# Kernel optimization log

Hardware: AMD Instinct MI355X
Metric: run time of the kernel (lower is better)

## Reference

```python
import jax, jax.numpy as jnp
import numpy as np

N_NODES, N_EDGES, D_FEAT, D_HID, K_CHEB = 30000, 480000, 256, 256, 2


def setup_inputs() -> dict:
    N, E, D, H, K = N_NODES, N_EDGES, D_FEAT, D_HID, K_CHEB
    key = jax.random.key(0)
    ks = jax.random.split(key, 24)
    sD = 1.0 / np.sqrt(D)
    sH = 1.0 / np.sqrt(H)
    inp = {
        "x": jax.random.normal(ks[0], (N, D), jnp.float32),
        "edge_index": jax.random.randint(ks[1], (2, E), 0, N),
        "edge_weight": jax.random.uniform(ks[2], (E,), jnp.float32),
        "h": jax.random.normal(ks[3], (N, H), jnp.float32),
        "c": jax.random.normal(ks[4], (N, H), jnp.float32),
        "src_neighbor_ids": jax.random.randint(ks[5], (E,), 0, N),
        "dst_neighbor_ids": jax.random.randint(ks[6], (E,), 0, N),
    }
    for j, nm in enumerate(["W_i", "W_f", "W_g", "W_o"]):
        inp[nm] = jax.random.normal(ks[7 + j], (D, H), jnp.float32) * sD
    for j, nm in enumerate(["Wc_i", "Wc_f", "Wc_g", "Wc_o"]):
        inp[nm] = jax.random.normal(ks[11 + j], (K, H, H), jnp.float32) * sH
    for nm in ["bc_i", "bc_f", "bc_g", "bc_o", "b_i", "b_f", "b_g", "b_o", "b_lin"]:
        inp[nm] = jnp.zeros((H,), jnp.float32)
    for j, nm in enumerate(["w_ci", "w_cf", "w_co"]):
        inp[nm] = jax.random.normal(ks[15 + j], (H,), jnp.float32) * 0.1
    inp["W_lin"] = jax.random.normal(ks[18], (H, H), jnp.float32) * sH
    return inp


def _cheb_conv(h, src, dst, norm, W, b):
    # ChebConv, K=2, sym norm, lambda_max=2: T0 = h, T1 = L_hat h = -D^-1/2 A D^-1/2 h
    out = h @ W[0]
    t1 = jax.ops.segment_sum(norm[:, None] * h[src], dst, num_segments=h.shape[0])
    return out + t1 @ W[1] + b


def reference(x, edge_index, edge_weight, h, c, src_neighbor_ids, dst_neighbor_ids,
              W_i, W_f, W_g, W_o, Wc_i, Wc_f, Wc_g, Wc_o,
              bc_i, bc_f, bc_g, bc_o, w_ci, w_cf, w_co,
              b_i, b_f, b_g, b_o, W_lin, b_lin):
    src, dst = edge_index[0], edge_index[1]
    n = x.shape[0]
    # neighbor-feature augmentation: gather both BEFORE any update, then scatter-add
    snf = x[src_neighbor_ids]
    dnf = x[dst_neighbor_ids]
    x = x.at[src].add(snf)
    x = x.at[dst].add(dnf)
    # symmetric Chebyshev normalization (lambda_max = 2 -> diagonal of L_hat is 0)
    deg = jax.ops.segment_sum(edge_weight, src, num_segments=n)
    dinv = jnp.where(deg > 0, jax.lax.rsqrt(jnp.maximum(deg, 1e-12)), 0.0)
    norm = -dinv[src] * edge_weight * dinv[dst]
    # GCLSTM gates
    i = jax.nn.sigmoid(x @ W_i + _cheb_conv(h, src, dst, norm, Wc_i, bc_i) + w_ci * c + b_i)
    f = jax.nn.sigmoid(x @ W_f + _cheb_conv(h, src, dst, norm, Wc_f, bc_f) + w_cf * c + b_f)
    g = jnp.tanh(x @ W_g + _cheb_conv(h, src, dst, norm, Wc_g, bc_g) + b_g)
    c_new = f * c + i * g
    o = jax.nn.sigmoid(x @ W_o + _cheb_conv(h, src, dst, norm, Wc_o, bc_o) + w_co * c_new + b_o)
    h0 = o * jnp.tanh(c_new)
    h_out = jax.nn.relu(h0) @ W_lin + b_lin
    return (h_out, h0, c_new)
```

## Files before the change

kernel.cpp:

```cpp
#include <hip/hip_runtime.h>
#include <math.h>

#define NN 30000
#define NE 480000
#define DH 256
#define NH (NN * DH)
#define MPAD 30080
#define CAP 64

typedef _Float16 f16x4 __attribute__((ext_vector_type(4)));
typedef _Float16 f16x8 __attribute__((ext_vector_type(8)));
typedef float f32x4 __attribute__((ext_vector_type(4)));

static __device__ __forceinline__ float sigmoidf_(float x) {
    return 1.0f / (1.0f + __expf(-x));
}

static __device__ __forceinline__ void gload16(const _Float16* g, _Float16* l) {
    __builtin_amdgcn_global_load_lds(
        (const __attribute__((address_space(1))) void*)g,
        (__attribute__((address_space(3))) void*)l, 16, 0, 0);
}


__global__ void prep0(const int* __restrict__ src, const float* __restrict__ ew,
                      float* __restrict__ deg,
                      const float* __restrict__ x, _Float16* __restrict__ x16,
                      const float* __restrict__ h, _Float16* __restrict__ h16) {
    int b = blockIdx.x;
    if (b < 1875) {
        int e = b * 256 + threadIdx.x;
        if (e < NE) atomicAdd(&deg[src[e]], ew[e]);
        return;
    }
    int i = (b - 1875) * 256 + threadIdx.x;
    const int n8 = NN * 32;
    const float* in; _Float16* out; int idx;
    if (i < n8) { in = x; out = x16; idx = i; }
    else if (i < 2 * n8) { in = h; out = h16; idx = i - n8; }
    else return;
    const float4 p = *reinterpret_cast<const float4*>(&in[(size_t)idx * 8]);
    const float4 q = *reinterpret_cast<const float4*>(&in[(size_t)idx * 8 + 4]);
    f16x8 v;
    v[0] = (_Float16)p.x; v[1] = (_Float16)p.y; v[2] = (_Float16)p.z; v[3] = (_Float16)p.w;
    v[4] = (_Float16)q.x; v[5] = (_Float16)q.y; v[6] = (_Float16)q.z; v[7] = (_Float16)q.w;
    *reinterpret_cast<f16x8*>(&out[(size_t)idx * 8]) = v;
}

__global__ void dinv_kernel(float* __restrict__ deg) {
    int v = blockIdx.x * blockDim.x + threadIdx.x;
    if (v < NN) {
        float d = deg[v];
        deg[v] = (d > 0.0f) ? rsqrtf(fmaxf(d, 1e-12f)) : 0.0f;
    }
}

__global__ void scatter2(const int* __restrict__ src, const int* __restrict__ dst,
                         const int* __restrict__ snf, const int* __restrict__ dnf,
                         const float* __restrict__ w, const float* __restrict__ dinv,
                         int* __restrict__ cntS, int* __restrict__ cntD,
                         int* __restrict__ slotS, int2* __restrict__ slotD) {
    int e = blockIdx.x * blockDim.x + threadIdx.x;
    if (e >= NE) return;
    int s = src[e], d = dst[e];
    int pS = atomicAdd(&cntS[s], 1);
    if (pS < CAP) slotS[s * CAP + pS] = snf[e];
    float nrm = -dinv[s] * w[e] * dinv[d];
    int pD = atomicAdd(&cntD[d], 1);
    if (pD < CAP) slotD[d * CAP + pD] = make_int2(s | (dnf[e] << 15), __float_as_int(nrm));
}

__global__ __launch_bounds__(256) void fused_gather(const _Float16* __restrict__ x16,
                                                    const _Float16* __restrict__ h16,
                                                    const int* __restrict__ cntS,
                                                    const int* __restrict__ cntD,
                                                    const int4* __restrict__ slotS4,
                                                    const int4* __restrict__ slotD4,
                                                    _Float16* __restrict__ A16) {
    int wid = (blockIdx.x * blockDim.x + threadIdx.x) >> 6;
    int l = threadIdx.x & 63;
    if (wid >= MPAD) return;
    size_t rb = (size_t)wid * 768;
    if (wid >= NN) {
        f16x4 z = {};
        *reinterpret_cast<f16x4*>(&A16[rb + l * 4]) = z;
        *reinterpret_cast<f16x4*>(&A16[rb + 256 + l * 4]) = z;
        *reinterpret_cast<f16x4*>(&A16[rb + 512 + l * 4]) = z;
        return;
    }
    int nS = min(cntS[wid], CAP);
    int nD = min(cntD[wid], CAP);

    f16x4 xv = *reinterpret_cast<const f16x4*>(&x16[(size_t)wid * 256 + l * 4]);
    f16x4 hrow = *reinterpret_cast<const f16x4*>(&h16[(size_t)wid * 256 + l * 4]);
    float a0 = (float)xv[0], a1 = (float)xv[1], a2 = (float)xv[2], a3 = (float)xv[3];
    float t0 = 0.f, t1 = 0.f, t2 = 0.f, t3 = 0.f;

    const int4* pS = &slotS4[(size_t)wid * (CAP / 4)];
    for (int j = 0; j < nS; j += 4) {
        int4 e = pS[j >> 2];
        f16x4 v0, v1, v2, v3;
        v0 = *reinterpret_cast<const f16x4*>(&x16[(size_t)e.x * 256 + l * 4]);
        if (j + 1 < nS) v1 = *reinterpret_cast<const f16x4*>(&x16[(size_t)e.y * 256 + l * 4]);
        if (j + 2 < nS) v2 = *reinterpret_cast<const f16x4*>(&x16[(size_t)e.z * 256 + l * 4]);
        if (j + 3 < nS) v3 = *reinterpret_cast<const f16x4*>(&x16[(size_t)e.w * 256 + l * 4]);
        a0 += (float)v0[0]; a1 += (float)v0[1]; a2 += (float)v0[2]; a3 += (float)v0[3];
        if (j + 1 < nS) { a0 += (float)v1[0]; a1 += (float)v1[1]; a2 += (float)v1[2]; a3 += (float)v1[3]; }
        if (j + 2 < nS) { a0 += (float)v2[0]; a1 += (float)v2[1]; a2 += (float)v2[2]; a3 += (float)v2[3]; }
        if (j + 3 < nS) { a0 += (float)v3[0]; a1 += (float)v3[1]; a2 += (float)v3[2]; a3 += (float)v3[3]; }
    }

    const int4* pD = &slotD4[(size_t)wid * (CAP / 2)];
    for (int j = 0; j < nD; j += 4) {
        int4 ea = pD[(j >> 2) * 2];
        int4 eb = pD[(j >> 2) * 2 + 1];
        int p0 = ea.x, p1 = ea.z, p2 = eb.x, p3 = eb.z;
        float n0 = __int_as_float(ea.y), n1f = __int_as_float(ea.w);
        float n2f = __int_as_float(eb.y), n3f = __int_as_float(eb.w);
        f16x4 x0, x1, x2, x3, g0, g1, g2, g3;
        x0 = *reinterpret_cast<const f16x4*>(&x16[(size_t)(p0 >> 15) * 256 + l * 4]);
        g0 = *reinterpret_cast<const f16x4*>(&h16[(size_t)(p0 & 0x7fff) * 256 + l * 4]);
        if (j + 1 < nD) {
            x1 = *reinterpret_cast<const f16x4*>(&x16[(size_t)(p1 >> 15) * 256 + l * 4]);
            g1 = *reinterpret_cast<const f16x4*>(&h16[(size_t)(p1 & 0x7fff) * 256 + l * 4]);
        }
        if (j + 2 < nD) {
            x2 = *reinterpret_cast<const f16x4*>(&x16[(size_t)(p2 >> 15) * 256 + l * 4]);
            g2 = *reinterpret_cast<const f16x4*>(&h16[(size_t)(p2 & 0x7fff) * 256 + l * 4]);
        }
        if (j + 3 < nD) {
            x3 = *reinterpret_cast<const f16x4*>(&x16[(size_t)(p3 >> 15) * 256 + l * 4]);
            g3 = *reinterpret_cast<const f16x4*>(&h16[(size_t)(p3 & 0x7fff) * 256 + l * 4]);
        }
        a0 += (float)x0[0]; a1 += (float)x0[1]; a2 += (float)x0[2]; a3 += (float)x0[3];
        t0 += n0 * (float)g0[0]; t1 += n0 * (float)g0[1];
        t2 += n0 * (float)g0[2]; t3 += n0 * (float)g0[3];
        if (j + 1 < nD) {
            a0 += (float)x1[0]; a1 += (float)x1[1]; a2 += (float)x1[2]; a3 += (float)x1[3];
            t0 += n1f * (float)g1[0]; t1 += n1f * (float)g1[1];
            t2 += n1f * (float)g1[2]; t3 += n1f * (float)g1[3];
        }
        if (j + 2 < nD) {
            a0 += (float)x2[0]; a1 += (float)x2[1]; a2 += (float)x2[2]; a3 += (float)x2[3];
            t0 += n2f * (float)g2[0]; t1 += n2f * (float)g2[1];
            t2 += n2f * (float)g2[2]; t3 += n2f * (float)g2[3];
        }
        if (j + 3 < nD) {
            a0 += (float)x3[0]; a1 += (float)x3[1]; a2 += (float)x3[2]; a3 += (float)x3[3];
            t0 += n3f * (float)g3[0]; t1 += n3f * (float)g3[1];
            t2 += n3f * (float)g3[2]; t3 += n3f * (float)g3[3];
        }
    }

    f16x4 oX, oT;
    oX[0] = (_Float16)a0; oX[1] = (_Float16)a1; oX[2] = (_Float16)a2; oX[3] = (_Float16)a3;
    oT[0] = (_Float16)t0; oT[1] = (_Float16)t1; oT[2] = (_Float16)t2; oT[3] = (_Float16)t3;
    *reinterpret_cast<f16x4*>(&A16[rb + l * 4]) = oX;
    *reinterpret_cast<f16x4*>(&A16[rb + 256 + l * 4]) = hrow;
    *reinterpret_cast<f16x4*>(&A16[rb + 512 + l * 4]) = oT;
}


__global__ void wpack_kernel(const float* __restrict__ W_i, const float* __restrict__ W_f,
                             const float* __restrict__ W_g, const float* __restrict__ W_o,
                             const float* __restrict__ Wc_i, const float* __restrict__ Wc_f,
                             const float* __restrict__ Wc_g, const float* __restrict__ Wc_o,
                             const float* __restrict__ W_lin,
                             _Float16* __restrict__ WcatT, _Float16* __restrict__ WlinT) {
    int idx = blockIdx.x * blockDim.x + threadIdx.x;
    if (idx < 768 * 1024) {
        int k = idx >> 10, n = idx & 1023;
        int seg = k >> 8, kk = k & 255, gate = n >> 8, nn = n & 255;
        const float* p;
        if (seg == 0) {
            p = (gate == 0) ? W_i : (gate == 1) ? W_f : (gate == 2) ? W_g : W_o;
        } else {
            const float* base = (gate == 0) ? Wc_i : (gate == 1) ? Wc_f : (gate == 2) ? Wc_g : Wc_o;
            p = base + (seg - 1) * 65536;
        }
        WcatT[(size_t)n * 768 + k] = (_Float16)p[kk * 256 + nn];
    } else {
        int i2 = idx - 768 * 1024;
        if (i2 >= 256 * 256) return;
        int k = i2 >> 8, n = i2 & 255;
        WlinT[(size_t)n * 256 + k] = (_Float16)W_lin[k * 256 + n];
    }
}


template <int K, int N, bool HALF_OUT, bool SWZ1D>
__global__ __launch_bounds__(256) void gemm16(const _Float16* __restrict__ A,
                                              const _Float16* __restrict__ B,
                                              const float* __restrict__ bias,
                                              _Float16* __restrict__ outH,
                                              float* __restrict__ outF) {
    __shared__ _Float16 As[128 * 64];
    __shared__ _Float16 Bs[128 * 64];
    int tid = threadIdx.x;
    int w = tid >> 6, l = tid & 63;
    int wy = w >> 1, wx = w & 1;
    int bm, bn;
    if constexpr (SWZ1D) {
        constexpr int NT = N / 128;
        constexpr int TOT = (MPAD / 128) * NT;
        constexpr int CH = TOT / 8;
        int b = blockIdx.x;
        int v = (b & 7) * CH + (b >> 3);
        bm = (v / NT) * 128; bn = (v % NT) * 128;
    } else {
        bm = blockIdx.x * 128; bn = blockIdx.y * 128;
    }

    f32x4 acc[4][4];
    #pragma unroll
    for (int m = 0; m < 4; ++m)
        #pragma unroll
        for (int n = 0; n < 4; ++n)
            acc[m][n] = (f32x4){0.f, 0.f, 0.f, 0.f};

    int rowi = tid >> 3;
    int g = (tid & 7) ^ (rowi & 7);
    const _Float16* gA0 = A + (size_t)(bm + rowi) * K + g * 8;
    const _Float16* gB0 = B + (size_t)(bn + rowi) * K + g * 8;

    for (int kt = 0; kt < K; kt += 64) {
        #pragma unroll
        for (int i = 0; i < 4; ++i) {
            gload16(gA0 + kt + (size_t)i * 32 * K, &As[i * 2048 + w * 512]);
            gload16(gB0 + kt + (size_t)i * 32 * K, &Bs[i * 2048 + w * 512]);
        }
        __syncthreads();

        f16x8 af[4][2], bf[4][2];
        #pragma unroll
        for (int m = 0; m < 4; ++m) {
            int row = wy * 64 + m * 16 + (l & 15);
            #pragma unroll
            for (int ks = 0; ks < 2; ++ks) {
                int ch = (ks * 4 + (l >> 4)) ^ (l & 7);
                af[m][ks] = *reinterpret_cast<const f16x8*>(&As[row * 64 + ch * 8]);
            }
        }
        #pragma unroll
        for (int n = 0; n < 4; ++n) {
            int row = wx * 64 + n * 16 + (l & 15);
            #pragma unroll
            for (int ks = 0; ks < 2; ++ks) {
                int ch = (ks * 4 + (l >> 4)) ^ (l & 7);
                bf[n][ks] = *reinterpret_cast<const f16x8*>(&Bs[row * 64 + ch * 8]);
            }
        }
        #pragma unroll
        for (int ks = 0; ks < 2; ++ks)
            #pragma unroll
            for (int m = 0; m < 4; ++m)
                #pragma unroll
                for (int n = 0; n < 4; ++n)
                    acc[m][n] = __builtin_amdgcn_mfma_f32_16x16x32_f16(
                        af[m][ks], bf[n][ks], acc[m][n], 0, 0, 0);
        __syncthreads();
    }

    #pragma unroll
    for (int m = 0; m < 4; ++m) {
        #pragma unroll
        for (int n = 0; n < 4; ++n) {
            int col = bn + wx * 64 + n * 16 + (l & 15);
            #pragma unroll
            for (int j = 0; j < 4; ++j) {
                int row = bm + wy * 64 + m * 16 + (l >> 4) * 4 + j;
                if (row < NN) {
                    if constexpr (HALF_OUT)
                        outH[(size_t)row * N + col] = (_Float16)acc[m][n][j];
                    else
                        outF[(size_t)row * N + col] = acc[m][n][j] + bias[col];
                }
            }
        }
    }
}


__global__ void gate_kernel(const _Float16* __restrict__ pre, const float* __restrict__ c,
                            const float* __restrict__ bc_i, const float* __restrict__ bc_f,
                            const float* __restrict__ bc_g, const float* __restrict__ bc_o,
                            const float* __restrict__ b_i, const float* __restrict__ b_f,
                            const float* __restrict__ b_g, const float* __restrict__ b_o,
                            const float* __restrict__ w_ci, const float* __restrict__ w_cf,
                            const float* __restrict__ w_co,
                            float* __restrict__ h0p, float* __restrict__ cnp,
                            _Float16* __restrict__ relu16) {
    int idx = blockIdx.x * blockDim.x + threadIdx.x;
    if (idx >= MPAD * 64) return;
    int row = idx >> 6;
    int n4 = (idx & 63) << 2;
    if (row >= NN) {
        f16x4 z = {};
        *reinterpret_cast<f16x4*>(&relu16[(size_t)row * 256 + n4]) = z;
        return;
    }
    size_t pb = (size_t)row * 1024;
    f16x4 pi = *reinterpret_cast<const f16x4*>(&pre[pb + n4]);
    f16x4 pf = *reinterpret_cast<const f16x4*>(&pre[pb + 256 + n4]);
    f16x4 pg = *reinterpret_cast<const f16x4*>(&pre[pb + 512 + n4]);
    f16x4 po = *reinterpret_cast<const f16x4*>(&pre[pb + 768 + n4]);
    float4 cv = *reinterpret_cast<const float4*>(&c[(size_t)row * 256 + n4]);
    float4 vbci = *reinterpret_cast<const float4*>(&bc_i[n4]);
    float4 vbcf = *reinterpret_cast<const float4*>(&bc_f[n4]);
    float4 vbcg = *reinterpret_cast<const float4*>(&bc_g[n4]);
    float4 vbco = *reinterpret_cast<const float4*>(&bc_o[n4]);
    float4 vbi  = *reinterpret_cast<const float4*>(&b_i[n4]);
    float4 vbf  = *reinterpret_cast<const float4*>(&b_f[n4]);
    float4 vbg  = *reinterpret_cast<const float4*>(&b_g[n4]);
    float4 vbo  = *reinterpret_cast<const float4*>(&b_o[n4]);
    float4 vwci = *reinterpret_cast<const float4*>(&w_ci[n4]);
    float4 vwcf = *reinterpret_cast<const float4*>(&w_cf[n4]);
    float4 vwco = *reinterpret_cast<const float4*>(&w_co[n4]);
    const float* CV = (const float*)&cv;
    const float* BCI = (const float*)&vbci; const float* BCF = (const float*)&vbcf;
    const float* BCG = (const float*)&vbcg; const float* BCO = (const float*)&vbco;
    const float* BI = (const float*)&vbi;   const float* BF = (const float*)&vbf;
    const float* BG = (const float*)&vbg;   const float* BO = (const float*)&vbo;
    const float* WCI = (const float*)&vwci; const float* WCF = (const float*)&vwcf;
    const float* WCO = (const float*)&vwco;
    float4 cn4, h04;
    float* CN = (float*)&cn4; float* H0 = (float*)&h04;
    f16x4 rl;
    #pragma unroll
    for (int j = 0; j < 4; ++j) {
        float iv = sigmoidf_((float)pi[j] + BCI[j] + BI[j] + WCI[j] * CV[j]);
        float fv = sigmoidf_((float)pf[j] + BCF[j] + BF[j] + WCF[j] * CV[j]);
        float gv = tanhf((float)pg[j] + BCG[j] + BG[j]);
        float cn = fv * CV[j] + iv * gv;
        float ov = sigmoidf_((float)po[j] + BCO[j] + BO[j] + WCO[j] * cn);
        CN[j] = cn;
        float h0 = ov * tanhf(cn);
        H0[j] = h0;
        rl[j] = (_Float16)fmaxf(h0, 0.f);
    }
    *reinterpret_cast<float4*>(&cnp[(size_t)row * 256 + n4]) = cn4;
    *reinterpret_cast<float4*>(&h0p[(size_t)row * 256 + n4]) = h04;
    *reinterpret_cast<f16x4*>(&relu16[(size_t)row * 256 + n4]) = rl;
}


extern "C" void kernel_launch(void* const* d_in, const int* in_sizes, int n_in,
                              void* d_out, int out_size, void* d_ws, size_t ws_size,
                              hipStream_t stream) {
    const float* x   = (const float*)d_in[0];
    const int*   ei  = (const int*)d_in[1];
    const float* ew  = (const float*)d_in[2];
    const float* h   = (const float*)d_in[3];
    const float* c   = (const float*)d_in[4];
    const int*   snf = (const int*)d_in[5];
    const int*   dnf = (const int*)d_in[6];
    const float* W_i = (const float*)d_in[7];
    const float* W_f = (const float*)d_in[8];
    const float* W_g = (const float*)d_in[9];
    const float* W_o = (const float*)d_in[10];
    const float* Wc_i = (const float*)d_in[11];
    const float* Wc_f = (const float*)d_in[12];
    const float* Wc_g = (const float*)d_in[13];
    const float* Wc_o = (const float*)d_in[14];
    const float* bc_i = (const float*)d_in[15];
    const float* bc_f = (const float*)d_in[16];
    const float* bc_g = (const float*)d_in[17];
    const float* bc_o = (const float*)d_in[18];
    const float* b_i  = (const float*)d_in[19];
    const float* b_f  = (const float*)d_in[20];
    const float* b_g  = (const float*)d_in[21];
    const float* b_o  = (const float*)d_in[22];
    const float* b_lin = (const float*)d_in[23];
    const float* w_ci = (const float*)d_in[24];
    const float* w_cf = (const float*)d_in[25];
    const float* w_co = (const float*)d_in[26];
    const float* W_lin = (const float*)d_in[27];

    const int* src = ei;
    const int* dst = ei + NE;

    float* out = (float*)d_out;
    float* houtp = out;
    float* h0p   = out + NH;
    float* cnp   = out + 2 * NH;

    char* ws = (char*)d_ws;
    _Float16* pre16 = (_Float16*)ws;
    int* cntS = (int*)ws;
    int* cntD = (int*)(ws + 131072);
    float* deg = (float*)(ws + 262144);
    int* slotS = (int*)(ws + 393216);
    int2* slotD = (int2*)(ws + 8073216);
    _Float16* h16 = (_Float16*)(ws + 23433216);

    _Float16* A16 = (_Float16*)(ws + 61440000);
    _Float16* A16lin = A16;
    _Float16* WcatT = (_Float16*)(ws + 107642880);
    _Float16* WlinT = (_Float16*)(ws + 109215744);
    _Float16* x16 = (_Float16*)(ws + 109346816);

    hipMemsetAsync(ws, 0, 393216, stream);

    prep0<<<9375, 256, 0, stream>>>(src, ew, deg, x, x16, h, h16);
    dinv_kernel<<<118, 256, 0, stream>>>(deg);

    scatter2<<<1875, 256, 0, stream>>>(src, dst, snf, dnf, ew, deg,
                                       cntS, cntD, slotS, slotD);

    fused_gather<<<7520, 256, 0, stream>>>(x16, h16, cntS, cntD,
                                           (const int4*)slotS, (const int4*)slotD, A16);

    wpack_kernel<<<3328, 256, 0, stream>>>(W_i, W_f, W_g, W_o, Wc_i, Wc_f, Wc_g, Wc_o,
                                           W_lin, WcatT, WlinT);

    gemm16<768, 1024, true, true><<<1880, 256, 0, stream>>>(A16, WcatT, nullptr, pre16, nullptr);

    gate_kernel<<<7520, 256, 0, stream>>>(pre16, c, bc_i, bc_f, bc_g, bc_o,
                                          b_i, b_f, b_g, b_o, w_ci, w_cf, w_co,
                                          h0p, cnp, A16lin);

    dim3 g2(MPAD / 128, 256 / 128);
    gemm16<256, 256, false, false><<<g2, 256, 0, stream>>>(A16lin, WlinT, b_lin, nullptr, houtp);
}
```

Before: 337.0 us.

## Fuse LSTM gate epilogue into the gate GEMM via interleaved weight columns

Reorders the packed gate weight columns so each output feature's i/f/g/o pre-activations sit next to each other, then computes the LSTM cell update inside the big GEMM's epilogue through a shared-memory staging tile. This drops the fp16 pre-activation buffer round trip through global memory and the separate gate kernel launch. Biases are pre-summed into a float4 table in the weight-pack kernel. The trade-off is a larger shared-memory footprint (which may cut occupancy) and an extra block-wide sync in the GEMM epilogue. Epilogue global stores are scalar per feature instead of vectorised.

```diff
diff --git a/kernel.cpp b/kernel.cpp
--- a/kernel.cpp
+++ b/kernel.cpp
@@ -69,6 +69,7 @@
     int pD = atomicAdd(&cntD[d], 1);
     if (pD < CAP) slotD[d * CAP + pD] = make_int2(s | (dnf[e] << 15), __float_as_int(nrm));
 }
+
 
 __global__ __launch_bounds__(256) void fused_gather(const _Float16* __restrict__ x16,
                                                     const _Float16* __restrict__ h16,
@@ -166,11 +167,18 @@
                              const float* __restrict__ Wc_i, const float* __restrict__ Wc_f,
                              const float* __restrict__ Wc_g, const float* __restrict__ Wc_o,
                              const float* __restrict__ W_lin,
-                             _Float16* __restrict__ WcatT, _Float16* __restrict__ WlinT) {
+                             const float* __restrict__ bc_i, const float* __restrict__ bc_f,
+                             const float* __restrict__ bc_g, const float* __restrict__ bc_o,
+                             const float* __restrict__ b_i, const float* __restrict__ b_f,
+                             const float* __restrict__ b_g, const float* __restrict__ b_o,
+                             const float* __restrict__ w_ci, const float* __restrict__ w_cf,
+                             const float* __restrict__ w_co,
+                             _Float16* __restrict__ WcatT, _Float16* __restrict__ WlinT,
+                             float4* __restrict__ bias4, float4* __restrict__ wc4) {
     int idx = blockIdx.x * blockDim.x + threadIdx.x;
     if (idx < 768 * 1024) {
         int k = idx >> 10, n = idx & 1023;
-        int seg = k >> 8, kk = k & 255, gate = n >> 8, nn = n & 255;
+        int seg = k >> 8, kk = k & 255, nn = n >> 2, gate = n & 3;
         const float* p;
         if (seg == 0) {
             p = (gate == 0) ? W_i : (gate == 1) ? W_f : (gate == 2) ? W_g : W_o;
@@ -179,23 +187,33 @@
             p = base + (seg - 1) * 65536;
         }
         WcatT[(size_t)n * 768 + k] = (_Float16)p[kk * 256 + nn];
-    } else {
+    } else if (idx < 768 * 1024 + 256 * 256) {
         int i2 = idx - 768 * 1024;
-        if (i2 >= 256 * 256) return;
         int k = i2 >> 8, n = i2 & 255;
         WlinT[(size_t)n * 256 + k] = (_Float16)W_lin[k * 256 + n];
-    }
-}
-
-
-template <int K, int N, bool HALF_OUT, bool SWZ1D>
+    } else if (idx < 768 * 1024 + 256 * 256 + 256) {
+        int f = idx - (768 * 1024 + 256 * 256);
+        bias4[f] = make_float4(bc_i[f] + b_i[f], bc_f[f] + b_f[f],
+                               bc_g[f] + b_g[f], bc_o[f] + b_o[f]);
+        wc4[f] = make_float4(w_ci[f], w_cf[f], w_co[f], 0.f);
+    }
+}
+
+
+template <int K, int N, int MODE, bool SWZ1D>
 __global__ __launch_bounds__(256) void gemm16(const _Float16* __restrict__ A,
                                               const _Float16* __restrict__ B,
                                               const float* __restrict__ bias,
-                                              _Float16* __restrict__ outH,
-                                              float* __restrict__ outF) {
-    __shared__ _Float16 As[128 * 64];
-    __shared__ _Float16 Bs[128 * 64];
+                                              float* __restrict__ outF,
+                                              const float* __restrict__ c,
+                                              const float4* __restrict__ bias4,
+                                              const float4* __restrict__ wc4,
+                                              float* __restrict__ h0p,
+                                              float* __restrict__ cnp,
+                                              _Float16* __restrict__ relu16) {
+    __shared__ _Float16 SH[128 * 132];
+    _Float16* As = SH;
+    _Float16* Bs = SH + 8192;
     int tid = threadIdx.x;
     int w = tid >> 6, l = tid & 63;
     int wy = w >> 1, wx = w & 1;
@@ -261,86 +279,61 @@
         __syncthreads();
     }
 
-    #pragma unroll
-    for (int m = 0; m < 4; ++m) {
-        #pragma unroll
-        for (int n = 0; n < 4; ++n) {
-            int col = bn + wx * 64 + n * 16 + (l & 15);
+    if constexpr (MODE == 0) {
+        #pragma unroll
+        for (int m = 0; m < 4; ++m) {
             #pragma unroll
-            for (int j = 0; j < 4; ++j) {
-                int row = bm + wy * 64 + m * 16 + (l >> 4) * 4 + j;
-                if (row < NN) {
-                    if constexpr (HALF_OUT)
-                        outH[(size_t)row * N + col] = (_Float16)acc[m][n][j];
-                    else
+            for (int n = 0; n < 4; ++n) {
+                int col = bn + wx * 64 + n * 16 + (l & 15);
+                #pragma unroll
+                for (int j = 0; j < 4; ++j) {
+                    int row = bm + wy * 64 + m * 16 + (l >> 4) * 4 + j;
+                    if (row < NN)
                         outF[(size_t)row * N + col] = acc[m][n][j] + bias[col];
                 }
             }
         }
-    }
-}
-
-
-__global__ void gate_kernel(const _Float16* __restrict__ pre, const float* __restrict__ c,
-                            const float* __restrict__ bc_i, const float* __restrict__ bc_f,
-                            const float* __restrict__ bc_g, const float* __restrict__ bc_o,
-                            const float* __restrict__ b_i, const float* __restrict__ b_f,
-                            const float* __restrict__ b_g, const float* __restrict__ b_o,
-                            const float* __restrict__ w_ci, const float* __restrict__ w_cf,
-                            const float* __restrict__ w_co,
-                            float* __restrict__ h0p, float* __restrict__ cnp,
-                            _Float16* __restrict__ relu16) {
-    int idx = blockIdx.x * blockDim.x + threadIdx.x;
-    if (idx >= MPAD * 64) return;
-    int row = idx >> 6;
-    int n4 = (idx & 63) << 2;
-    if (row >= NN) {
-        f16x4 z = {};
-        *reinterpret_cast<f16x4*>(&relu16[(size_t)row * 256 + n4]) = z;
-        return;
-    }
-    size_t pb = (size_t)row * 1024;
-    f16x4 pi = *reinterpret_cast<const f16x4*>(&pre[pb + n4]);
-    f16x4 pf = *reinterpret_cast<const f16x4*>(&pre[pb + 256 + n4]);
-    f16x4 pg = *reinterpret_cast<const f16x4*>(&pre[pb + 512 + n4]);
-    f16x4 po = *reinterpret_cast<const f16x4*>(&pre[pb + 768 + n4]);
-    float4 cv = *reinterpret_cast<const float4*>(&c[(size_t)row * 256 + n4]);
-    float4 vbci = *reinterpret_cast<const float4*>(&bc_i[n4]);
-    float4 vbcf = *reinterpret_cast<const float4*>(&bc_f[n4]);
-    float4 vbcg = *reinterpret_cast<const float4*>(&bc_g[n4]);
-    float4 vbco = *reinterpret_cast<const float4*>(&bc_o[n4]);
-    float4 vbi  = *reinterpret_cast<const float4*>(&b_i[n4]);
-    float4 vbf  = *reinterpret_cast<const float4*>(&b_f[n4]);
-    float4 vbg  = *reinterpret_cast<const float4*>(&b_g[n4]);
-    float4 vbo  = *reinterpret_cast<const float4*>(&b_o[n4]);
-    float4 vwci = *reinterpret_cast<const float4*>(&w_ci[n4]);
-    float4 vwcf = *reinterpret_cast<const float4*>(&w_cf[n4]);
-    float4 vwco = *reinterpret_cast<const float4*>(&w_co[n4]);
-    const float* CV = (const float*)&cv;
-    const float* BCI = (const float*)&vbci; const float* BCF = (const float*)&vbcf;
-    const float* BCG = (const float*)&vbcg; const float* BCO = (const float*)&vbco;
-    const float* BI = (const float*)&vbi;   const float* BF = (const float*)&vbf;
-    const float* BG = (const float*)&vbg;   const float* BO = (const float*)&vbo;
-    const float* WCI = (const float*)&vwci; const float* WCF = (const float*)&vwcf;
-    const float* WCO = (const float*)&vwco;
-    float4 cn4, h04;
-    float* CN = (float*)&cn4; float* H0 = (float*)&h04;
-    f16x4 rl;
-    #pragma unroll
-    for (int j = 0; j < 4; ++j) {
-        float iv = sigmoidf_((float)pi[j] + BCI[j] + BI[j] + WCI[j] * CV[j]);
-        float fv = sigmoidf_((float)pf[j] + BCF[j] + BF[j] + WCF[j] * CV[j]);
-        float gv = tanhf((float)pg[j] + BCG[j] + BG[j]);
-        float cn = fv * CV[j] + iv * gv;
-        float ov = sigmoidf_((float)po[j] + BCO[j] + BO[j] + WCO[j] * cn);
-        CN[j] = cn;
-        float h0 = ov * tanhf(cn);
-        H0[j] = h0;
-        rl[j] = (_Float16)fmaxf(h0, 0.f);
-    }
-    *reinterpret_cast<float4*>(&cnp[(size_t)row * 256 + n4]) = cn4;
-    *reinterpret_cast<float4*>(&h0p[(size_t)row * 256 + n4]) = h04;
-    *reinterpret_cast<f16x4*>(&relu16[(size_t)row * 256 + n4]) = rl;
+    } else {
+        #pragma unroll
+        for (int m = 0; m < 4; ++m) {
+            #pragma unroll
+            for (int n = 0; n < 4; ++n) {
+                int col_l = wx * 64 + n * 16 + (l & 15);
+                #pragma unroll
+                for (int j = 0; j < 4; ++j) {
+                    int row_l = wy * 64 + m * 16 + (l >> 4) * 4 + j;
+                    SH[row_l * 132 + col_l] = (_Float16)acc[m][n][j];
+                }
+            }
+        }
+        __syncthreads();
+        int fb = bn >> 2;
+        int feat_l = tid & 31;
+        int f = fb + feat_l;
+        int rb_ = (tid >> 5) * 16;
+        float4 b4 = bias4[f];
+        float4 w4 = wc4[f];
+        #pragma unroll
+        for (int i = 0; i < 16; ++i) {
+            int row_l = rb_ + i;
+            int grow = bm + row_l;
+            f16x4 pv = *reinterpret_cast<const f16x4*>(&SH[row_l * 132 + feat_l * 4]);
+            if (grow < NN) {
+                float cv = c[(size_t)grow * 256 + f];
+                float iv = sigmoidf_((float)pv[0] + b4.x + w4.x * cv);
+                float fv = sigmoidf_((float)pv[1] + b4.y + w4.y * cv);
+                float gv = tanhf((float)pv[2] + b4.z);
+                float cn = fv * cv + iv * gv;
+                float ov = sigmoidf_((float)pv[3] + b4.w + w4.z * cn);
+                float h0 = ov * tanhf(cn);
+                cnp[(size_t)grow * 256 + f] = cn;
+                h0p[(size_t)grow * 256 + f] = h0;
+                relu16[(size_t)grow * 256 + f] = (_Float16)fmaxf(h0, 0.f);
+            } else {
+                relu16[(size_t)grow * 256 + f] = (_Float16)0.f;
+            }
+        }
+    }
 }
 
 
@@ -385,19 +378,20 @@
     float* cnp   = out + 2 * NH;
 
     char* ws = (char*)d_ws;
-    _Float16* pre16 = (_Float16*)ws;
     int* cntS = (int*)ws;
     int* cntD = (int*)(ws + 131072);
     float* deg = (float*)(ws + 262144);
     int* slotS = (int*)(ws + 393216);
     int2* slotD = (int2*)(ws + 8073216);
     _Float16* h16 = (_Float16*)(ws + 23433216);
+    _Float16* relu16 = (_Float16*)ws;
 
     _Float16* A16 = (_Float16*)(ws + 61440000);
-    _Float16* A16lin = A16;
     _Float16* WcatT = (_Float16*)(ws + 107642880);
     _Float16* WlinT = (_Float16*)(ws + 109215744);
-    _Float16* x16 = (_Float16*)(ws + 109346816);
+    float4* bias4 = (float4*)(ws + 109346816);
+    float4* wc4 = (float4*)(ws + 109350912);
+    _Float16* x16 = (_Float16*)(ws + 109477888);
 
     hipMemsetAsync(ws, 0, 393216, stream);
 
@@ -410,15 +404,15 @@
     fused_gather<<<7520, 256, 0, stream>>>(x16, h16, cntS, cntD,
                                            (const int4*)slotS, (const int4*)slotD, A16);
 
-    wpack_kernel<<<3328, 256, 0, stream>>>(W_i, W_f, W_g, W_o, Wc_i, Wc_f, Wc_g, Wc_o,
-                                           W_lin, WcatT, WlinT);
-
-    gemm16<768, 1024, true, true><<<1880, 256, 0, stream>>>(A16, WcatT, nullptr, pre16, nullptr);
-
-    gate_kernel<<<7520, 256, 0, stream>>>(pre16, c, bc_i, bc_f, bc_g, bc_o,
-                                          b_i, b_f, b_g, b_o, w_ci, w_cf, w_co,
-                                          h0p, cnp, A16lin);
+    wpack_kernel<<<3329, 256, 0, stream>>>(W_i, W_f, W_g, W_o, Wc_i, Wc_f, Wc_g, Wc_o,
+                                           W_lin, bc_i, bc_f, bc_g, bc_o,
+                                           b_i, b_f, b_g, b_o, w_ci, w_cf, w_co,
+                                           WcatT, WlinT, bias4, wc4);
+
+    gemm16<768, 1024, 1, true><<<1880, 256, 0, stream>>>(
+        A16, WcatT, nullptr, nullptr, c, bias4, wc4, h0p, cnp, relu16);
 
     dim3 g2(MPAD / 128, 256 / 128);
-    gemm16<256, 256, false, false><<<g2, 256, 0, stream>>>(A16lin, WlinT, b_lin, nullptr, houtp);
-}
+    gemm16<256, 256, 0, false><<<g2, 256, 0, stream>>>(
+        relu16, WlinT, b_lin, houtp, nullptr, nullptr, nullptr, nullptr, nullptr, nullptr);
+}
```

After: 347.3 us. 3.0% more time.
